# Optimization experiments

Hardware: AMD Instinct MI355X
Metric: run time of the kernel (lower is better)

Reference implementation:

```python
import jax, jax.numpy as jnp
import numpy as np

N = 100_000      # num nodes
E = 100_000      # num hyperedges
NNZ = 1_600_000  # incidence entries (avg degree 16)
DIN = 128
DOUT = 128


def setup_inputs() -> dict:
    key = jax.random.key(0)
    k1, k2, k3, k4 = jax.random.split(key, 4)
    x = jax.random.normal(k1, (N, DIN), dtype=jnp.float32)
    weight = jax.random.normal(k2, (DIN, DOUT), dtype=jnp.float32) / np.sqrt(DIN).astype(np.float32)
    bias = jax.random.normal(k3, (DOUT,), dtype=jnp.float32) * 0.02
    hyperedge_index = jax.random.randint(k4, (2, NNZ), 0, N, dtype=jnp.int64)
    return {"x": x, "weight": weight, "bias": bias, "hyperedge_index": hyperedge_index}


def reference(x, weight, bias, hyperedge_index):
    # PyG HypergraphConv (use_attention=False, heads=1):
    #   out = D^{-1} H W B^{-1} H^T (x @ Theta) + bias, W = I (unit hyperedge weights)
    node_idx = hyperedge_index[0]  # [NNZ]
    edge_idx = hyperedge_index[1]  # [NNZ]

    h = x @ weight  # [N, DOUT]

    ones = jnp.ones((NNZ,), dtype=h.dtype)
    # node degree D_i = sum of hyperedge weights (=1) over incident hyperedges
    D = jax.ops.segment_sum(ones, node_idx, num_segments=N)   # [N]
    # hyperedge degree B_e = number of incident nodes
    B = jax.ops.segment_sum(ones, edge_idx, num_segments=E)   # [E]
    Dinv = jnp.where(D > 0, 1.0 / D, 0.0)
    Binv = jnp.where(B > 0, 1.0 / B, 0.0)

    # nodes -> hyperedges: m_e = B_e^{-1} * sum_{i in e} h_i
    e_feat = jax.ops.segment_sum(h[node_idx], edge_idx, num_segments=E) * Binv[:, None]  # [E, DOUT]
    # hyperedges -> nodes: out_i = D_i^{-1} * sum_{e ni i} m_e
    out = jax.ops.segment_sum(e_feat[edge_idx], node_idx, num_segments=N) * Dinv[:, None]  # [N, DOUT]
    return out + bias
```

## Files before the change

### kernel.cpp

```cpp
#include <hip/hip_runtime.h>

#define Nn 100000
#define Ne 100000
#define NNZC 1600000
#define NBLK 256
#define CHUNK 6250
#define BSH 8
#define BUCKW 256
#define NBK 391
#define CAPB 5120
#define GEMM_TOTAL 391
#define FCAP 4608
#define SEGW 4
#define NG0 6250

typedef __attribute__((ext_vector_type(8))) short short8;
typedef __attribute__((ext_vector_type(4))) float floatx4;

__device__ inline unsigned short f2bf(float f) {
    union { float f; unsigned int i; } c; c.f = f;
    unsigned int i = c.i;
    return (unsigned short)((i + 0x7fffu + ((i >> 16) & 1u)) >> 16);
}
__device__ inline unsigned int f2bf2(float lo, float hi) {
    union { float f; unsigned int i; } a, b;
    a.f = lo; b.f = hi;
    const unsigned int x = (a.i + 0x7fffu + ((a.i >> 16) & 1u)) >> 16;
    const unsigned int y = (b.i + 0x7fffu + ((b.i >> 16) & 1u)) & 0xffff0000u;
    return x | y;
}

struct FineLds {
    int cnt[BUCKW];
    int tmp[2][BUCKW];
    unsigned int cache[FCAP];
};
union FineGemmLds {
    unsigned short wlds[128 * 136];
    FineLds f;
};

__device__ inline void gemm_block256(int gb, const float* __restrict__ x,
                                     const float* __restrict__ w,
                                     unsigned short* __restrict__ h,
                                     unsigned short* wlds, int tid) {
    const int wave = tid >> 6, lane = tid & 63;
    const int q = lane >> 4, r16 = lane & 15;

    for (int i = tid; i < 4096; i += 256) {
        const int k = i >> 5;
        const int n0 = (i & 31) << 2;
        const float4 wv = *(const float4*)(w + k * 128 + n0);
        wlds[(n0 + 0) * 136 + k] = f2bf(wv.x);
        wlds[(n0 + 1) * 136 + k] = f2bf(wv.y);
        wlds[(n0 + 2) * 136 + k] = f2bf(wv.z);
        wlds[(n0 + 3) * 136 + k] = f2bf(wv.w);
    }
    __syncthreads();

#pragma unroll 1
    for (int rg = 0; rg < 4; ++rg) {
        const int row0 = gb * 256 + rg * 64 + wave * 16;
        const int rrow = min(row0 + r16, Nn - 1);

        floatx4 acc[8];
#pragma unroll
        for (int jb = 0; jb < 8; ++jb) acc[jb] = (floatx4){0.f, 0.f, 0.f, 0.f};

        const float* ap = x + (size_t)rrow * 128 + q * 8;
#pragma unroll
        for (int kk = 0; kk < 4; ++kk) {
            const float4 a0 = *(const float4*)(ap + kk * 32);
            const float4 a1 = *(const float4*)(ap + kk * 32 + 4);
            union { unsigned int u[4]; short8 s; } xf;
            xf.u[0] = f2bf2(a0.x, a0.y);
            xf.u[1] = f2bf2(a0.z, a0.w);
            xf.u[2] = f2bf2(a1.x, a1.y);
            xf.u[3] = f2bf2(a1.z, a1.w);
            const unsigned short* wp = wlds + kk * 32 + q * 8;
#pragma unroll
            for (int jb = 0; jb < 8; ++jb) {
                const short8 wf = *(const short8*)(wp + (jb * 16 + r16) * 136);
                acc[jb] = __builtin_amdgcn_mfma_f32_16x16x32_bf16(wf, xf.s, acc[jb], 0, 0, 0);
            }
        }

        if (row0 + r16 < Nn) {
            unsigned short* hb = h + (size_t)(row0 + r16) * 128 + q * 4;
#pragma unroll
            for (int jb = 0; jb < 8; ++jb) {
                uint2 o;
                o.x = f2bf2(acc[jb][0], acc[jb][1]);
                o.y = f2bf2(acc[jb][2], acc[jb][3]);
                *(uint2*)(hb + jb * 16) = o;
            }
        }
    }
}

__global__ __launch_bounds__(256) void scatter_kernel(
        const int* __restrict__ nidx, const int* __restrict__ eidx,
        int* __restrict__ gcurN, int* __restrict__ gcurE,
        unsigned int* __restrict__ pairsN, unsigned int* __restrict__ pairsE) {
    __shared__ struct { int a[NBK]; int b[NBK]; } sm;
    const int tid = threadIdx.x;
    for (int j = tid; j < NBK; j += 256) { sm.a[j] = 0; sm.b[j] = 0; }
    __syncthreads();
    const int base = blockIdx.x * CHUNK;
    for (int i = base + tid; i < base + CHUNK; i += 256) {
        atomicAdd(&sm.a[nidx[i] >> BSH], 1);
        atomicAdd(&sm.b[eidx[i] >> BSH], 1);
    }
    __syncthreads();
    for (int j = tid; j < NBK; j += 256) {
        sm.a[j] = atomicAdd(&gcurN[j], sm.a[j]);
        sm.b[j] = atomicAdd(&gcurE[j], sm.b[j]);
    }
    __syncthreads();
    for (int i = base + tid; i < base + CHUNK; i += 256) {
        const int n = nidx[i], e = eidx[i];
        const int pn = atomicAdd(&sm.a[n >> BSH], 1);
        if (pn < CAPB)
            pairsN[(size_t)(n >> BSH) * CAPB + pn] =
                ((unsigned int)e << 8) | (unsigned int)(n & 255);
        const int pe = atomicAdd(&sm.b[e >> BSH], 1);
        if (pe < CAPB)
            pairsE[(size_t)(e >> BSH) * CAPB + pe] =
                ((unsigned int)n << 8) | (unsigned int)(e & 255);
    }
}

__device__ inline void fine_block(int b, const unsigned int* __restrict__ pairs,
                                  const int* __restrict__ gcur,
                                  int* __restrict__ offs, int* __restrict__ perm,
                                  FineLds& L, int t) {
    const int cnt_b = min(gcur[b], CAPB);
    int part = 0;
    for (int j = t; j < b; j += 256) part += min(gcur[j], CAPB);
    L.tmp[0][t] = part;
    __syncthreads();
    for (int off = 128; off > 0; off >>= 1) {
        if (t < off) L.tmp[0][t] += L.tmp[0][t + off];
        __syncthreads();
    }
    const int S = L.tmp[0][0];
    __syncthreads();

    const unsigned int* pb = pairs + (size_t)b * CAPB;
    L.cnt[t] = 0;
    __syncthreads();
    for (int i = t; i < cnt_b; i += BUCKW) {
        const unsigned int p = pb[i];
        if (i < FCAP) L.cache[i] = p;
        atomicAdd(&L.cnt[p & 255u], 1);
    }
    __syncthreads();
    int v = L.cnt[t];
    int pin = 0;
    L.tmp[0][t] = v;
    for (int off = 1; off < BUCKW; off <<= 1) {
        __syncthreads();
        int val = L.tmp[pin][t];
        if (t >= off) val += L.tmp[pin][t - off];
        L.tmp[1 - pin][t] = val;
        pin ^= 1;
    }
    __syncthreads();
    const int excl = L.tmp[pin][t] - v;
    const int id = b * BUCKW + t;
    if (id < 100000) offs[id] = S + excl;
    if (b == NBK - 1 && t == 0) offs[100000] = NNZC;
    __syncthreads();
    L.cnt[t] = excl;
    __syncthreads();
    for (int i = t; i < cnt_b; i += BUCKW) {
        const unsigned int p = (i < FCAP) ? L.cache[i] : pb[i];
        const int pos = S + atomicAdd(&L.cnt[p & 255u], 1);
        perm[pos] = (int)(p >> 8);
    }
}

template <int MODE>
__device__ inline void gather_body(int gblk, const int* __restrict__ perm,
                                   const int* __restrict__ offs,
                                   const void* __restrict__ srcv,
                                   const float* __restrict__ bias,
                                   void* __restrict__ outv, int tid) {
    const int wave = tid >> 6;
    const int lane = tid & 63;
    const int e0 = __builtin_amdgcn_readfirstlane((gblk * 4 + wave) * SEGW);
    const int start = offs[e0];
    const int end = offs[e0 + SEGW];
    const unsigned int laneoff = (unsigned int)lane << 2;
    const char* src = (const char*)srcv;

    float bx = 0.f, by = 0.f;
    if (MODE == 1) {
        const float2 b = ((const float2*)bias)[lane];
        bx = b.x; by = b.y;
    }

    float ax = 0.f, ay = 0.f;
    int e = e0;
    int seg_start = start;
    int nb = offs[e0 + 1];

    auto flush = [&](int deg) {
        const float sinv = deg ? 1.f / (float)deg : 0.f;
        if (MODE == 0) {
            *(unsigned int*)((char*)outv + (((unsigned int)e << 8) | laneoff)) =
                f2bf2(ax * sinv, ay * sinv);
        } else {
            float2 o;
            o.x = ax * sinv + bx;
            o.y = ay * sinv + by;
            *(float2*)((char*)outv + (((unsigned int)e << 9) | (laneoff << 1))) = o;
        }
        ax = 0.f; ay = 0.f;
        ++e;
    };

    int myv = 0;
    for (int i = start; i < end; i += 8) {
        const int t = (i - start) & 63;
        if (t == 0) myv = perm[min(i + lane, NNZC - 1)];
        const int m = min(end - i, 8);
        unsigned int a[8], u[8];
#pragma unroll
        for (int j = 0; j < 8; ++j)
            a[j] = ((unsigned int)__shfl(myv, t + (j < m ? j : m - 1), 64) << 8) | laneoff;
#pragma unroll
        for (int j = 0; j < 8; ++j) u[j] = *(const unsigned int*)(src + a[j]);
#pragma unroll
        for (int j = 0; j < 8; ++j) {
            if (j < m) {
                while (i + j == nb) {
                    flush(nb - seg_start);
                    seg_start = nb;
                    nb = offs[e + 1];
                }
                ax += __uint_as_float(u[j] << 16);
                ay += __uint_as_float(u[j] & 0xffff0000u);
            }
        }
    }
    while (e < e0 + SEGW) {
        flush(end - seg_start);
        seg_start = end;
    }
}

__global__ __launch_bounds__(256) void gemmE_kernel(
        const float* __restrict__ x, const float* __restrict__ w,
        unsigned short* __restrict__ h,
        const unsigned int* __restrict__ pairsE, const int* __restrict__ gcurE,
        int* __restrict__ offsE, int* __restrict__ permE) {
    __shared__ FineGemmLds sm;
    const int tid = threadIdx.x;
    if (blockIdx.x < GEMM_TOTAL) {
        gemm_block256(blockIdx.x, x, w, h, sm.wlds, tid);
    } else {
        fine_block(blockIdx.x - GEMM_TOTAL, pairsE, gcurE, offsE, permE, sm.f, tid);
    }
}

__global__ __launch_bounds__(256) void g0_fineN_kernel(
        const int* __restrict__ permE, const int* __restrict__ offsE,
        const unsigned short* __restrict__ h, unsigned short* __restrict__ ef,
        const unsigned int* __restrict__ pairsN, const int* __restrict__ gcurN,
        int* __restrict__ offsN, int* __restrict__ permN) {
    __shared__ FineLds sm;
    const int tid = threadIdx.x;
    if (blockIdx.x < NBK) {
        fine_block(blockIdx.x, pairsN, gcurN, offsN, permN, sm, tid);
    } else {
        gather_body<0>(blockIdx.x - NBK, permE, offsE, h, nullptr, ef, tid);
    }
}

__global__ __launch_bounds__(256) void gather_e2n_kernel(
        const int* __restrict__ permN, const int* __restrict__ offsN,
        const unsigned short* __restrict__ ef, const float* __restrict__ bias,
        float* __restrict__ out) {
    gather_body<1>(blockIdx.x, permN, offsN, ef, bias, out, threadIdx.x);
}

extern "C" void kernel_launch(void* const* d_in, const int* in_sizes, int n_in,
                              void* d_out, int out_size, void* d_ws, size_t ws_size,
                              hipStream_t stream) {
    const float* x = (const float*)d_in[0];
    const float* w = (const float*)d_in[1];
    const float* bias = (const float*)d_in[2];
    const int* hei = (const int*)d_in[3];
    const int* nidx = hei;
    const int* eidx = hei + NNZC;
    float* out = (float*)d_out;

    char* p = (char*)d_ws;
    unsigned short* h = (unsigned short*)p;  p += (size_t)Nn * 128 * 2;
    unsigned short* ef = (unsigned short*)p; p += (size_t)Ne * 128 * 2;
    int* gcurN = (int*)p;                    p += NBK * 4 + 192;
    int* gcurE = (int*)p;                    p += NBK * 4 + 192;
    int* offsN = (int*)p;                    p += 400128;
    int* offsE = (int*)p;                    p += 400128;
    int* permN = (int*)p;                    p += (size_t)NNZC * 4;
    int* permE = (int*)p;                    p += (size_t)NNZC * 4;
    unsigned int* pairsN = (unsigned int*)p; p += (size_t)NBK * CAPB * 4;
    unsigned int* pairsE = (unsigned int*)p; p += (size_t)NBK * CAPB * 4;

    hipMemsetAsync(gcurN, 0, 2 * (NBK * 4 + 192), stream);

    scatter_kernel<<<NBLK, 256, 0, stream>>>(nidx, eidx, gcurN, gcurE, pairsN, pairsE);
    gemmE_kernel<<<GEMM_TOTAL + NBK, 256, 0, stream>>>(x, w, h, pairsE, gcurE,
                                                       offsE, permE);
    g0_fineN_kernel<<<NBK + NG0, 256, 0, stream>>>(permE, offsE, h, ef,
                                                   pairsN, gcurN, offsN, permN);
    gather_e2n_kernel<<<NG0, 256, 0, stream>>>(permN, offsN, ef, bias, out);
}
```

Measured before the change: 297.1 us.

## Rebalance grid: finer scatter chunks, 64-row GEMM blocks, both fine sorts in one kernel

Splits the scatter pass into 2048 smaller chunks so more blocks run concurrently. The GEMM now uses 64-row blocks (1563 of them), and that kernel also runs the node-side and edge-side fine bucket sorts. The first gather becomes its own kernel instead of sharing a launch with the node fine sort. The aim is better GPU occupancy and load balance across the pipeline stages. The cost is more global atomics in scatter, a weight reload and bf16 conversion per 64 rows, and the node→edge gather can no longer overlap with the node fine sort.

```diff
diff --git a/kernel.cpp b/kernel.cpp
--- a/kernel.cpp
+++ b/kernel.cpp
@@ -3,13 +3,13 @@
 #define Nn 100000
 #define Ne 100000
 #define NNZC 1600000
-#define NBLK 256
-#define CHUNK 6250
+#define NBLK 2048
+#define CHUNK 782
 #define BSH 8
 #define BUCKW 256
 #define NBK 391
 #define CAPB 5120
-#define GEMM_TOTAL 391
+#define GEMM_TOTAL 1563
 #define FCAP 4608
 #define SEGW 4
 #define NG0 6250
@@ -35,68 +35,10 @@
     int tmp[2][BUCKW];
     unsigned int cache[FCAP];
 };
-union FineGemmLds {
+union GemmFineLds {
     unsigned short wlds[128 * 136];
     FineLds f;
 };
-
-__device__ inline void gemm_block256(int gb, const float* __restrict__ x,
-                                     const float* __restrict__ w,
-                                     unsigned short* __restrict__ h,
-                                     unsigned short* wlds, int tid) {
-    const int wave = tid >> 6, lane = tid & 63;
-    const int q = lane >> 4, r16 = lane & 15;
-
-    for (int i = tid; i < 4096; i += 256) {
-        const int k = i >> 5;
-        const int n0 = (i & 31) << 2;
-        const float4 wv = *(const float4*)(w + k * 128 + n0);
-        wlds[(n0 + 0) * 136 + k] = f2bf(wv.x);
-        wlds[(n0 + 1) * 136 + k] = f2bf(wv.y);
-        wlds[(n0 + 2) * 136 + k] = f2bf(wv.z);
-        wlds[(n0 + 3) * 136 + k] = f2bf(wv.w);
-    }
-    __syncthreads();
-
-#pragma unroll 1
-    for (int rg = 0; rg < 4; ++rg) {
-        const int row0 = gb * 256 + rg * 64 + wave * 16;
-        const int rrow = min(row0 + r16, Nn - 1);
-
-        floatx4 acc[8];
-#pragma unroll
-        for (int jb = 0; jb < 8; ++jb) acc[jb] = (floatx4){0.f, 0.f, 0.f, 0.f};
-
-        const float* ap = x + (size_t)rrow * 128 + q * 8;
-#pragma unroll
-        for (int kk = 0; kk < 4; ++kk) {
-            const float4 a0 = *(const float4*)(ap + kk * 32);
-            const float4 a1 = *(const float4*)(ap + kk * 32 + 4);
-            union { unsigned int u[4]; short8 s; } xf;
-            xf.u[0] = f2bf2(a0.x, a0.y);
-            xf.u[1] = f2bf2(a0.z, a0.w);
-            xf.u[2] = f2bf2(a1.x, a1.y);
-            xf.u[3] = f2bf2(a1.z, a1.w);
-            const unsigned short* wp = wlds + kk * 32 + q * 8;
-#pragma unroll
-            for (int jb = 0; jb < 8; ++jb) {
-                const short8 wf = *(const short8*)(wp + (jb * 16 + r16) * 136);
-                acc[jb] = __builtin_amdgcn_mfma_f32_16x16x32_bf16(wf, xf.s, acc[jb], 0, 0, 0);
-            }
-        }
-
-        if (row0 + r16 < Nn) {
-            unsigned short* hb = h + (size_t)(row0 + r16) * 128 + q * 4;
-#pragma unroll
-            for (int jb = 0; jb < 8; ++jb) {
-                uint2 o;
-                o.x = f2bf2(acc[jb][0], acc[jb][1]);
-                o.y = f2bf2(acc[jb][2], acc[jb][3]);
-                *(uint2*)(hb + jb * 16) = o;
-            }
-        }
-    }
-}
 
 __global__ __launch_bounds__(256) void scatter_kernel(
         const int* __restrict__ nidx, const int* __restrict__ eidx,
@@ -107,7 +49,8 @@
     for (int j = tid; j < NBK; j += 256) { sm.a[j] = 0; sm.b[j] = 0; }
     __syncthreads();
     const int base = blockIdx.x * CHUNK;
-    for (int i = base + tid; i < base + CHUNK; i += 256) {
+    const int lim = min(base + CHUNK, NNZC);
+    for (int i = base + tid; i < lim; i += 256) {
         atomicAdd(&sm.a[nidx[i] >> BSH], 1);
         atomicAdd(&sm.b[eidx[i] >> BSH], 1);
     }
@@ -117,7 +60,7 @@
         sm.b[j] = atomicAdd(&gcurE[j], sm.b[j]);
     }
     __syncthreads();
-    for (int i = base + tid; i < base + CHUNK; i += 256) {
+    for (int i = base + tid; i < lim; i += 256) {
         const int n = nidx[i], e = eidx[i];
         const int pn = atomicAdd(&sm.a[n >> BSH], 1);
         if (pn < CAPB)
@@ -130,6 +73,61 @@
     }
 }
 
+__device__ inline void gemm_block64(int gb, const float* __restrict__ x,
+                                    const float* __restrict__ w,
+                                    unsigned short* __restrict__ h,
+                                    unsigned short* wlds, int tid) {
+    const int wave = tid >> 6, lane = tid & 63;
+    const int q = lane >> 4, r16 = lane & 15;
+
+    for (int i = tid; i < 4096; i += 256) {
+        const int k = i >> 5;
+        const int n0 = (i & 31) << 2;
+        const float4 wv = *(const float4*)(w + k * 128 + n0);
+        wlds[(n0 + 0) * 136 + k] = f2bf(wv.x);
+        wlds[(n0 + 1) * 136 + k] = f2bf(wv.y);
+        wlds[(n0 + 2) * 136 + k] = f2bf(wv.z);
+        wlds[(n0 + 3) * 136 + k] = f2bf(wv.w);
+    }
+    __syncthreads();
+
+    const int row0 = gb * 64 + wave * 16;
+    const int rrow = min(row0 + r16, Nn - 1);
+
+    floatx4 acc[8];
+#pragma unroll
+    for (int jb = 0; jb < 8; ++jb) acc[jb] = (floatx4){0.f, 0.f, 0.f, 0.f};
+
+    const float* ap = x + (size_t)rrow * 128 + q * 8;
+#pragma unroll
+    for (int kk = 0; kk < 4; ++kk) {
+        const float4 a0 = *(const float4*)(ap + kk * 32);
+        const float4 a1 = *(const float4*)(ap + kk * 32 + 4);
+        union { unsigned int u[4]; short8 s; } xf;
+        xf.u[0] = f2bf2(a0.x, a0.y);
+        xf.u[1] = f2bf2(a0.z, a0.w);
+        xf.u[2] = f2bf2(a1.x, a1.y);
+        xf.u[3] = f2bf2(a1.z, a1.w);
+        const unsigned short* wp = wlds + kk * 32 + q * 8;
+#pragma unroll
+        for (int jb = 0; jb < 8; ++jb) {
+            const short8 wf = *(const short8*)(wp + (jb * 16 + r16) * 136);
+            acc[jb] = __builtin_amdgcn_mfma_f32_16x16x32_bf16(wf, xf.s, acc[jb], 0, 0, 0);
+        }
+    }
+
+    if (row0 + r16 < Nn) {
+        unsigned short* hb = h + (size_t)(row0 + r16) * 128 + q * 4;
+#pragma unroll
+        for (int jb = 0; jb < 8; ++jb) {
+            uint2 o;
+            o.x = f2bf2(acc[jb][0], acc[jb][1]);
+            o.y = f2bf2(acc[jb][2], acc[jb][3]);
+            *(uint2*)(hb + jb * 16) = o;
+        }
+    }
+}
+
 __device__ inline void fine_block(int b, const unsigned int* __restrict__ pairs,
                                   const int* __restrict__ gcur,
                                   int* __restrict__ offs, int* __restrict__ perm,
@@ -177,6 +175,25 @@
         const unsigned int p = (i < FCAP) ? L.cache[i] : pb[i];
         const int pos = S + atomicAdd(&L.cnt[p & 255u], 1);
         perm[pos] = (int)(p >> 8);
+    }
+}
+
+__global__ __launch_bounds__(256) void gemmfine_kernel(
+        const float* __restrict__ x, const float* __restrict__ w,
+        unsigned short* __restrict__ h,
+        const unsigned int* __restrict__ pairsE, const int* __restrict__ gcurE,
+        int* __restrict__ offsE, int* __restrict__ permE,
+        const unsigned int* __restrict__ pairsN, const int* __restrict__ gcurN,
+        int* __restrict__ offsN, int* __restrict__ permN) {
+    __shared__ GemmFineLds sm;
+    const int tid = threadIdx.x;
+    const int vb = blockIdx.x;
+    if (vb < GEMM_TOTAL) {
+        gemm_block64(vb, x, w, h, sm.wlds, tid);
+    } else if (vb < GEMM_TOTAL + NBK) {
+        fine_block(vb - GEMM_TOTAL, pairsE, gcurE, offsE, permE, sm.f, tid);
+    } else {
+        fine_block(vb - GEMM_TOTAL - NBK, pairsN, gcurN, offsN, permN, sm.f, tid);
     }
 }
 
@@ -250,32 +267,10 @@
     }
 }
 
-__global__ __launch_bounds__(256) void gemmE_kernel(
-        const float* __restrict__ x, const float* __restrict__ w,
-        unsigned short* __restrict__ h,
-        const unsigned int* __restrict__ pairsE, const int* __restrict__ gcurE,
-        int* __restrict__ offsE, int* __restrict__ permE) {
-    __shared__ FineGemmLds sm;
-    const int tid = threadIdx.x;
-    if (blockIdx.x < GEMM_TOTAL) {
-        gemm_block256(blockIdx.x, x, w, h, sm.wlds, tid);
-    } else {
-        fine_block(blockIdx.x - GEMM_TOTAL, pairsE, gcurE, offsE, permE, sm.f, tid);
-    }
-}
-
-__global__ __launch_bounds__(256) void g0_fineN_kernel(
+__global__ __launch_bounds__(256) void gather_n2e_kernel(
         const int* __restrict__ permE, const int* __restrict__ offsE,
-        const unsigned short* __restrict__ h, unsigned short* __restrict__ ef,
-        const unsigned int* __restrict__ pairsN, const int* __restrict__ gcurN,
-        int* __restrict__ offsN, int* __restrict__ permN) {
-    __shared__ FineLds sm;
-    const int tid = threadIdx.x;
-    if (blockIdx.x < NBK) {
-        fine_block(blockIdx.x, pairsN, gcurN, offsN, permN, sm, tid);
-    } else {
-        gather_body<0>(blockIdx.x - NBK, permE, offsE, h, nullptr, ef, tid);
-    }
+        const unsigned short* __restrict__ h, unsigned short* __restrict__ ef) {
+    gather_body<0>(blockIdx.x, permE, offsE, h, nullptr, ef, threadIdx.x);
 }
 
 __global__ __launch_bounds__(256) void gather_e2n_kernel(
@@ -311,9 +306,9 @@
     hipMemsetAsync(gcurN, 0, 2 * (NBK * 4 + 192), stream);
 
     scatter_kernel<<<NBLK, 256, 0, stream>>>(nidx, eidx, gcurN, gcurE, pairsN, pairsE);
-    gemmE_kernel<<<GEMM_TOTAL + NBK, 256, 0, stream>>>(x, w, h, pairsE, gcurE,
-                                                       offsE, permE);
-    g0_fineN_kernel<<<NBK + NG0, 256, 0, stream>>>(permE, offsE, h, ef,
-                                                   pairsN, gcurN, offsN, permN);
+    gemmfine_kernel<<<GEMM_TOTAL + 2 * NBK, 256, 0, stream>>>(x, w, h,
+                                                              pairsE, gcurE, offsE, permE,
+                                                              pairsN, gcurN, offsN, permN);
+    gather_n2e_kernel<<<NG0, 256, 0, stream>>>(permE, offsE, h, ef);
     gather_e2n_kernel<<<NG0, 256, 0, stream>>>(permN, offsN, ef, bias, out);
 }
```

Measured after the change: 371.8 us. +25.1%, slower.
